# Optimization experiments

Hardware: AMD Instinct MI355X
Metric: run time of the kernel (lower is better)

Reference implementation:

```python
import jax, jax.numpy as jnp
import numpy as np

ENC_D, PRED_D, JOINT_D, VOCAB = 256, 256, 512, 1024

def setup_inputs() -> dict:
    key = jax.random.key(0)
    ks = jax.random.split(key, 8)
    B, T, U = 4, 256, 64
    s = lambda d: 1.0 / np.sqrt(d)
    return {
        "encoder_outputs": jax.random.normal(ks[0], (B, T, ENC_D), jnp.float32),
        "predictor_outputs": jax.random.normal(ks[1], (B, U, PRED_D), jnp.float32),
        "W_enc": jax.random.uniform(ks[2], (ENC_D, JOINT_D), jnp.float32, -s(ENC_D), s(ENC_D)),
        "b_enc": jax.random.uniform(ks[3], (JOINT_D,), jnp.float32, -s(ENC_D), s(ENC_D)),
        "W_dec": jax.random.uniform(ks[4], (PRED_D, JOINT_D), jnp.float32, -s(PRED_D), s(PRED_D)),
        "b_dec": jax.random.uniform(ks[5], (JOINT_D,), jnp.float32, -s(PRED_D), s(PRED_D)),
        "W_out": jax.random.uniform(ks[6], (JOINT_D, VOCAB), jnp.float32, -s(JOINT_D), s(JOINT_D)),
        "b_out": jax.random.uniform(ks[7], (VOCAB,), jnp.float32, -s(JOINT_D), s(JOINT_D)),
    }

def reference(encoder_outputs, predictor_outputs, W_enc, b_enc, W_dec, b_dec, W_out, b_out):
    # [B,T,J] and [B,U,J] projections
    enc = jnp.einsum('bte,ej->btj', encoder_outputs, W_enc) + b_enc
    pred = jnp.einsum('bup,pj->buj', predictor_outputs, W_dec) + b_dec
    # broadcast add -> [B,T,U,J], tanh, then output projection -> [B,T,U,V]
    joint = jnp.tanh(enc[:, :, None, :] + pred[:, None, :, :])
    logits = jnp.einsum('btuj,jv->btuv', joint, W_out) + b_out
    return logits
```

## Files before the change

kernel.cpp:

```cpp
#include <hip/hip_runtime.h>
#include <hip/hip_bf16.h>

typedef __attribute__((ext_vector_type(8))) short bf16x8;
typedef __attribute__((ext_vector_type(4))) float fvec4;
typedef __attribute__((ext_vector_type(16))) float f32x16;
typedef __attribute__((ext_vector_type(8))) unsigned short u16x8;


__device__ __forceinline__ unsigned short f2bf(float f) {
  unsigned int u = __builtin_bit_cast(unsigned int, f);
  u += 0x7FFFu + ((u >> 16) & 1u);
  return (unsigned short)(u >> 16);
}

__device__ __forceinline__ float fast_tanh(float x) {
  float cx = fminf(fmaxf(x, -9.0f), 9.0f);
  float e2 = __expf(cx + cx);
  return (e2 - 1.0f) * __builtin_amdgcn_rcpf(e2 + 1.0f);
}


__device__ __forceinline__ void proj_body(
    const float* __restrict__ x, const float* __restrict__ W,
    const float* __restrict__ bias, float* __restrict__ out,
    int blk, uint8_t* sh) {
  float (*xt)[9] = (float (*)[9])sh;
  const int tid = threadIdx.x;
  const int row0 = blk << 3;
  #pragma unroll
  for (int i = 0; i < 8; ++i)
    xt[tid][i] = x[(size_t)(row0 + i) * 256 + tid];
  __syncthreads();
  float acc0[8] = {0.f,0.f,0.f,0.f,0.f,0.f,0.f,0.f};
  float acc1[8] = {0.f,0.f,0.f,0.f,0.f,0.f,0.f,0.f};
  #pragma unroll 4
  for (int k = 0; k < 256; ++k) {
    float w0 = W[(size_t)k * 512 + tid];
    float w1 = W[(size_t)k * 512 + tid + 256];
    #pragma unroll
    for (int r = 0; r < 8; ++r) {
      float xv = xt[k][r];
      acc0[r] = fmaf(xv, w0, acc0[r]);
      acc1[r] = fmaf(xv, w1, acc1[r]);
    }
  }
  float b0 = bias[tid], b1 = bias[tid + 256];
  #pragma unroll
  for (int r = 0; r < 8; ++r) {
    out[(size_t)(row0 + r) * 512 + tid]       = acc0[r] + b0;
    out[(size_t)(row0 + r) * 512 + tid + 256] = acc1[r] + b1;
  }
}

__device__ __forceinline__ void transpose_body(
    const float* __restrict__ W, unsigned short* __restrict__ Bt3,
    int blk, uint8_t* sh) {
  unsigned short (*tile)[65] = (unsigned short (*)[65])sh;
  const int k0 = (blk & 7) << 6;
  const int n0 = (blk >> 3) << 6;
  const int tid = threadIdx.x;
  #pragma unroll
  for (int i = 0; i < 16; ++i) {
    int idx = tid + (i << 8);
    int r = idx >> 6, c = idx & 63;
    tile[r][c] = f2bf(W[(size_t)(k0 + r) * 1024 + n0 + c]);
  }
  __syncthreads();
  #pragma unroll
  for (int i = 0; i < 16; ++i) {
    int idx = tid + (i << 8);
    int r = idx >> 6, c = idx & 63;
    int ng = n0 + r, kg = k0 + c;
    size_t dst = ((size_t)(ng >> 9) << 18) + ((size_t)(kg >> 4) << 13)
               + ((ng & 511) << 4) + (kg & 15);
    Bt3[dst] = tile[c][r];
  }
}

__global__ __launch_bounds__(256) void prep_kernel(
    const float* __restrict__ enc, const float* __restrict__ We,
    const float* __restrict__ be, float* __restrict__ encp,
    const float* __restrict__ pred, const float* __restrict__ Wd,
    const float* __restrict__ bd, float* __restrict__ predp,
    const float* __restrict__ Wo, unsigned short* __restrict__ Bt3) {
  __shared__ uint8_t sh[9216];
  const int b = blockIdx.x;
  if (b < 128)       proj_body(enc, We, be, encp, b, sh);
  else if (b < 160)  proj_body(pred, Wd, bd, predp, b - 128, sh);
  else               transpose_body(Wo, Bt3, b - 160, sh);
}

__global__ __launch_bounds__(512, 4) void fused_gemm(
    const float* __restrict__ encp, const float* __restrict__ predp,
    const unsigned short* __restrict__ Bt3, const float* __restrict__ bout,
    float* __restrict__ out) {
  __shared__ uint8_t lds[66560];
  const int tid = threadIdx.x;
  const int lane = tid & 63, wid = tid >> 6;
  const int l31 = lane & 31, hi = lane >> 5;
  const int b = blockIdx.x;
  const int wg = ((b & 7) << 8) + (b >> 3);
  const int mt = wg >> 1, half = wg & 1;
  const int m0 = mt << 6;
  const int cb0 = half << 9;

  const unsigned short* Bgl =
      Bt3 + ((size_t)half << 18) + (((wid << 6) + l31) << 4) + (hi << 3);

  bf16x8 bA[2], bB[2];
  #pragma unroll
  for (int na = 0; na < 2; ++na)
    bA[na] = *(const bf16x8*)(Bgl + (na << 9));

  {
    const int r = tid >> 3, cb = tid & 7;
    const float* erow = encp + ((size_t)mt << 9);
    const float* prow = predp + ((size_t)(((mt >> 8) << 6) + r) << 9);
    uint8_t* rowbase = lds + (r << 10);
    #pragma unroll
    for (int c8 = 0; c8 < 8; ++c8) {
      int chunk = cb + (c8 << 3);
      int k8 = chunk << 3;
      fvec4 e0 = *(const fvec4*)(erow + k8);
      fvec4 e1 = *(const fvec4*)(erow + k8 + 4);
      fvec4 p0 = *(const fvec4*)(prow + k8);
      fvec4 p1 = *(const fvec4*)(prow + k8 + 4);
      u16x8 o;
      #pragma unroll
      for (int i = 0; i < 4; ++i) o[i]     = f2bf(fast_tanh(e0[i] + p0[i]));
      #pragma unroll
      for (int i = 0; i < 4; ++i) o[i + 4] = f2bf(fast_tanh(e1[i] + p1[i]));
      *(u16x8*)(rowbase + ((chunk ^ (r & 15)) << 4)) = o;
    }
  }
  asm volatile("s_waitcnt lgkmcnt(0)" ::: "memory");
  __builtin_amdgcn_s_barrier();

  f32x16 acc[2][2];
  #pragma unroll
  for (int i = 0; i < 2; ++i)
    #pragma unroll
    for (int j = 0; j < 2; ++j)
      #pragma unroll
      for (int e = 0; e < 16; ++e) acc[i][j][e] = 0.f;

  const int hx = hi ^ (lane & 15);
  int arowb[2];
  #pragma unroll
  for (int ma = 0; ma < 2; ++ma)
    arowb[ma] = ((ma << 5) + l31) << 10;

  auto step = [&](int kt, bf16x8 (&cur)[2], bf16x8 (&nxt)[2]) {
    const int ktn = kt < 31 ? kt + 1 : 31;
    #pragma unroll
    for (int na = 0; na < 2; ++na)
      nxt[na] = *(const bf16x8*)(Bgl + (ktn << 13) + (na << 9));
    const int ao = (((kt << 1) ^ hx) << 4);
    bf16x8 af[2];
    #pragma unroll
    for (int ma = 0; ma < 2; ++ma)
      af[ma] = *(const bf16x8*)(lds + arowb[ma] + ao);
    #pragma unroll
    for (int ma = 0; ma < 2; ++ma)
      #pragma unroll
      for (int na = 0; na < 2; ++na)
        acc[ma][na] = __builtin_amdgcn_mfma_f32_32x32x16_bf16(
            cur[na], af[ma], acc[ma][na], 0, 0, 0);
  };

  #pragma unroll
  for (int kt = 0; kt < 32; kt += 2) {
    step(kt,     bA, bB);
    step(kt + 1, bB, bA);
  }

  float (*epi)[516] = (float (*)[516])lds;
  fvec4 bvv[2][4];
  #pragma unroll
  for (int na = 0; na < 2; ++na)
    #pragma unroll
    for (int q = 0; q < 4; ++q)
      bvv[na][q] = *(const fvec4*)&bout[cb0 + (wid << 6) + (na << 5) +
                                       (q << 3) + (hi << 2)];

  #pragma unroll
  for (int ma = 0; ma < 2; ++ma) {
    asm volatile("s_waitcnt lgkmcnt(0)" ::: "memory");
    __builtin_amdgcn_s_barrier();
    #pragma unroll
    for (int na = 0; na < 2; ++na)
      #pragma unroll
      for (int q = 0; q < 4; ++q) {
        fvec4 o;
        #pragma unroll
        for (int j = 0; j < 4; ++j) o[j] = acc[ma][na][(q << 2) + j] + bvv[na][q][j];
        *(fvec4*)&epi[l31][(wid << 6) + (na << 5) + (q << 3) + (hi << 2)] = o;
      }
    asm volatile("s_waitcnt lgkmcnt(0)" ::: "memory");
    __builtin_amdgcn_s_barrier();
    #pragma unroll
    for (int j = 0; j < 8; ++j) {
      const int idx = (wid << 3) + j;
      const int row = idx >> 1, seg = idx & 1;
      fvec4 v = *(const fvec4*)&epi[row][(seg << 8) + (lane << 2)];
      const int gm = m0 + (ma << 5) + row;
      __builtin_nontemporal_store(
          v, (fvec4*)&out[(size_t)gm * 1024 + cb0 + (seg << 8) + (lane << 2)]);
    }
  }
}

extern "C" void kernel_launch(void* const* d_in, const int* in_sizes, int n_in,
                              void* d_out, int out_size, void* d_ws, size_t ws_size,
                              hipStream_t stream) {
  const float* enc   = (const float*)d_in[0];
  const float* pred  = (const float*)d_in[1];
  const float* W_enc = (const float*)d_in[2];
  const float* b_enc = (const float*)d_in[3];
  const float* W_dec = (const float*)d_in[4];
  const float* b_dec = (const float*)d_in[5];
  const float* W_out = (const float*)d_in[6];
  const float* b_out = (const float*)d_in[7];
  float* out = (float*)d_out;

  uint8_t* ws = (uint8_t*)d_ws;
  float* encp  = (float*)ws;
  float* predp = (float*)(ws + 2097152);
  unsigned short* bt3 = (unsigned short*)(ws + 2621440);

  prep_kernel<<<288, 256, 0, stream>>>(enc, W_enc, b_enc, encp,
                                       pred, W_dec, b_dec, predp,
                                       W_out, bt3);
  fused_gemm<<<2048, 512, 0, stream>>>(encp, predp, bt3, b_out, out);
}
```

Before: 126.3 us.

## Shrink GEMM tile to 64x128 and split A build into two K halves

Output tile per workgroup drops from 64x512 to 64x128, with each wave computing one 32x32 accumulator instead of a 2x2 set, and the grid grows from 2048 to 8192 blocks. The tanh-joint A tile is built in two K halves of 256 so LDS use falls to about 34KB, and launch bounds now ask for 8 blocks per CU. The aim is higher occupancy and lower register pressure to hide latency. The cost is rebuilding the joint tile once per 128-column tile, four times as often as before, plus less register reuse of B and A fragments and extra barriers.

```diff
diff --git a/kernel.cpp b/kernel.cpp
--- a/kernel.cpp
+++ b/kernel.cpp
@@ -90,35 +90,35 @@
   else               transpose_body(Wo, Bt3, b - 160, sh);
 }
 
-__global__ __launch_bounds__(512, 4) void fused_gemm(
+__global__ __launch_bounds__(512, 8) void fused_gemm(
     const float* __restrict__ encp, const float* __restrict__ predp,
     const unsigned short* __restrict__ Bt3, const float* __restrict__ bout,
     float* __restrict__ out) {
-  __shared__ uint8_t lds[66560];
+  __shared__ uint8_t lds[34816];
   const int tid = threadIdx.x;
   const int lane = tid & 63, wid = tid >> 6;
   const int l31 = lane & 31, hi = lane >> 5;
+  const int wm = wid >> 2, wn = wid & 3;
   const int b = blockIdx.x;
-  const int wg = ((b & 7) << 8) + (b >> 3);
-  const int mt = wg >> 1, half = wg & 1;
+  const int wg = ((b & 7) << 10) + (b >> 3);
+  const int mt = wg >> 3, nt = wg & 7;
   const int m0 = mt << 6;
-  const int cb0 = half << 9;
+  const int n0 = nt << 7;
+  const int half = nt >> 2;
 
   const unsigned short* Bgl =
-      Bt3 + ((size_t)half << 18) + (((wid << 6) + l31) << 4) + (hi << 3);
-
-  bf16x8 bA[2], bB[2];
-  #pragma unroll
-  for (int na = 0; na < 2; ++na)
-    bA[na] = *(const bf16x8*)(Bgl + (na << 9));
-
-  {
+      Bt3 + ((size_t)half << 18) + ((((nt & 3) << 7) + (wn << 5) + l31) << 4) + (hi << 3);
+
+  bf16x8 bA, bB;
+  bA = *(const bf16x8*)(Bgl);
+
+  auto build_A = [&](int h) {
     const int r = tid >> 3, cb = tid & 7;
-    const float* erow = encp + ((size_t)mt << 9);
-    const float* prow = predp + ((size_t)(((mt >> 8) << 6) + r) << 9);
-    uint8_t* rowbase = lds + (r << 10);
+    const float* erow = encp + ((size_t)mt << 9) + (h << 8);
+    const float* prow = predp + ((size_t)(((mt >> 8) << 6) + r) << 9) + (h << 8);
+    uint8_t* rowbase = lds + (r << 9);
     #pragma unroll
-    for (int c8 = 0; c8 < 8; ++c8) {
+    for (int c8 = 0; c8 < 4; ++c8) {
       int chunk = cb + (c8 << 3);
       int k8 = chunk << 3;
       fvec4 e0 = *(const fvec4*)(erow + k8);
@@ -132,81 +132,64 @@
       for (int i = 0; i < 4; ++i) o[i + 4] = f2bf(fast_tanh(e1[i] + p1[i]));
       *(u16x8*)(rowbase + ((chunk ^ (r & 15)) << 4)) = o;
     }
-  }
-  asm volatile("s_waitcnt lgkmcnt(0)" ::: "memory");
-  __builtin_amdgcn_s_barrier();
-
-  f32x16 acc[2][2];
-  #pragma unroll
-  for (int i = 0; i < 2; ++i)
-    #pragma unroll
-    for (int j = 0; j < 2; ++j)
-      #pragma unroll
-      for (int e = 0; e < 16; ++e) acc[i][j][e] = 0.f;
-
-  const int hx = hi ^ (lane & 15);
-  int arowb[2];
-  #pragma unroll
-  for (int ma = 0; ma < 2; ++ma)
-    arowb[ma] = ((ma << 5) + l31) << 10;
-
-  auto step = [&](int kt, bf16x8 (&cur)[2], bf16x8 (&nxt)[2]) {
+  };
+
+  build_A(0);
+  asm volatile("s_waitcnt lgkmcnt(0)" ::: "memory");
+  __builtin_amdgcn_s_barrier();
+
+  f32x16 acc;
+  #pragma unroll
+  for (int e = 0; e < 16; ++e) acc[e] = 0.f;
+
+  const int arow = (wm << 5) + l31;
+  const int abase = arow << 9;
+  const int am = arow & 15;
+
+  auto step = [&](int kt, bf16x8& cur, bf16x8& nxt) {
     const int ktn = kt < 31 ? kt + 1 : 31;
-    #pragma unroll
-    for (int na = 0; na < 2; ++na)
-      nxt[na] = *(const bf16x8*)(Bgl + (ktn << 13) + (na << 9));
-    const int ao = (((kt << 1) ^ hx) << 4);
-    bf16x8 af[2];
-    #pragma unroll
-    for (int ma = 0; ma < 2; ++ma)
-      af[ma] = *(const bf16x8*)(lds + arowb[ma] + ao);
-    #pragma unroll
-    for (int ma = 0; ma < 2; ++ma)
-      #pragma unroll
-      for (int na = 0; na < 2; ++na)
-        acc[ma][na] = __builtin_amdgcn_mfma_f32_32x32x16_bf16(
-            cur[na], af[ma], acc[ma][na], 0, 0, 0);
+    nxt = *(const bf16x8*)(Bgl + (ktn << 13));
+    const int ktl = kt & 15;
+    bf16x8 af = *(const bf16x8*)(lds + abase + ((((ktl << 1) | hi) ^ am) << 4));
+    acc = __builtin_amdgcn_mfma_f32_32x32x16_bf16(cur, af, acc, 0, 0, 0);
   };
 
   #pragma unroll
-  for (int kt = 0; kt < 32; kt += 2) {
+  for (int kt = 0; kt < 16; kt += 2) {
     step(kt,     bA, bB);
     step(kt + 1, bB, bA);
   }
-
-  float (*epi)[516] = (float (*)[516])lds;
-  fvec4 bvv[2][4];
-  #pragma unroll
-  for (int na = 0; na < 2; ++na)
+  asm volatile("s_waitcnt lgkmcnt(0)" ::: "memory");
+  __builtin_amdgcn_s_barrier();
+  build_A(1);
+  asm volatile("s_waitcnt lgkmcnt(0)" ::: "memory");
+  __builtin_amdgcn_s_barrier();
+  #pragma unroll
+  for (int kt = 16; kt < 32; kt += 2) {
+    step(kt,     bA, bB);
+    step(kt + 1, bB, bA);
+  }
+
+  float (*epi)[133] = (float (*)[133])lds;
+  asm volatile("s_waitcnt lgkmcnt(0)" ::: "memory");
+  __builtin_amdgcn_s_barrier();
+  #pragma unroll
+  for (int q = 0; q < 4; ++q) {
+    const int col = (wn << 5) + (q << 3) + (hi << 2);
+    fvec4 bv = *(const fvec4*)&bout[n0 + col];
+    fvec4 o;
     #pragma unroll
-    for (int q = 0; q < 4; ++q)
-      bvv[na][q] = *(const fvec4*)&bout[cb0 + (wid << 6) + (na << 5) +
-                                       (q << 3) + (hi << 2)];
-
-  #pragma unroll
-  for (int ma = 0; ma < 2; ++ma) {
-    asm volatile("s_waitcnt lgkmcnt(0)" ::: "memory");
-    __builtin_amdgcn_s_barrier();
-    #pragma unroll
-    for (int na = 0; na < 2; ++na)
-      #pragma unroll
-      for (int q = 0; q < 4; ++q) {
-        fvec4 o;
-        #pragma unroll
-        for (int j = 0; j < 4; ++j) o[j] = acc[ma][na][(q << 2) + j] + bvv[na][q][j];
-        *(fvec4*)&epi[l31][(wid << 6) + (na << 5) + (q << 3) + (hi << 2)] = o;
-      }
-    asm volatile("s_waitcnt lgkmcnt(0)" ::: "memory");
-    __builtin_amdgcn_s_barrier();
-    #pragma unroll
-    for (int j = 0; j < 8; ++j) {
-      const int idx = (wid << 3) + j;
-      const int row = idx >> 1, seg = idx & 1;
-      fvec4 v = *(const fvec4*)&epi[row][(seg << 8) + (lane << 2)];
-      const int gm = m0 + (ma << 5) + row;
-      __builtin_nontemporal_store(
-          v, (fvec4*)&out[(size_t)gm * 1024 + cb0 + (seg << 8) + (lane << 2)]);
-    }
+    for (int j = 0; j < 4; ++j) o[j] = acc[(q << 2) + j] + bv[j];
+    *(fvec4*)&epi[(wm << 5) + l31][col] = o;
+  }
+  asm volatile("s_waitcnt lgkmcnt(0)" ::: "memory");
+  __builtin_amdgcn_s_barrier();
+  #pragma unroll
+  for (int j = 0; j < 4; ++j) {
+    const int row = (wid << 3) + (j << 1) + hi;
+    fvec4 v = *(const fvec4*)&epi[row][l31 << 2];
+    __builtin_nontemporal_store(
+        v, (fvec4*)&out[(size_t)(m0 + row) * 1024 + n0 + (l31 << 2)]);
   }
 }
 
@@ -231,5 +214,5 @@
   prep_kernel<<<288, 256, 0, stream>>>(enc, W_enc, b_enc, encp,
                                        pred, W_dec, b_dec, predp,
                                        W_out, bt3);
-  fused_gemm<<<2048, 512, 0, stream>>>(encp, predp, bt3, b_out, out);
-}
+  fused_gemm<<<8192, 512, 0, stream>>>(encp, predp, bt3, b_out, out);
+}
```

After: 231.3 us. 83.1% more time.

## Split tanh joint computation into separate kernel writing bf16 A tiles

Applied to the files above, without the earlier changes.

Moves the broadcast-add, tanh and bf16 conversion out of the GEMM into a standalone joint_kernel that writes the full [B*T*U, 512] bf16 activation matrix to workspace in an MFMA-friendly layout. The GEMM then streams A fragments straight from global memory with register double-buffering instead of building them in LDS behind a barrier. This removes the duplicated tanh work (each A row was recomputed by both column halves) and the LDS prologue stall. In exchange it adds an extra launch and a large activation round trip through HBM (about 64 MB written and read back).

```diff
diff --git a/kernel.cpp b/kernel.cpp
--- a/kernel.cpp
+++ b/kernel.cpp
@@ -90,11 +90,38 @@
   else               transpose_body(Wo, Bt3, b - 160, sh);
 }
 
-__global__ __launch_bounds__(512, 4) void fused_gemm(
+__global__ __launch_bounds__(256) void joint_kernel(
     const float* __restrict__ encp, const float* __restrict__ predp,
-    const unsigned short* __restrict__ Bt3, const float* __restrict__ bout,
-    float* __restrict__ out) {
-  __shared__ uint8_t lds[66560];
+    unsigned short* __restrict__ Aj) {
+  const int vid = blockIdx.x * 256 + threadIdx.x;
+  const int r = vid & 31;
+  const int s = vid >> 5;
+  const int kt = s & 31;
+  const int g = s >> 5;
+  const int k0 = kt << 4;
+  const float* e = encp + ((size_t)(g >> 1) << 9) + k0;
+  const float* p = predp + (((size_t)((g >> 9) << 6) + ((g & 1) << 5) + r) << 9) + k0;
+  fvec4 ev0 = *(const fvec4*)e,        ev1 = *(const fvec4*)(e + 4);
+  fvec4 ev2 = *(const fvec4*)(e + 8),  ev3 = *(const fvec4*)(e + 12);
+  fvec4 pv0 = *(const fvec4*)p,        pv1 = *(const fvec4*)(p + 4);
+  fvec4 pv2 = *(const fvec4*)(p + 8),  pv3 = *(const fvec4*)(p + 12);
+  u16x8 o0, o1;
+  #pragma unroll
+  for (int i = 0; i < 4; ++i) {
+    o0[i]     = f2bf(fast_tanh(ev0[i] + pv0[i]));
+    o0[i + 4] = f2bf(fast_tanh(ev1[i] + pv1[i]));
+    o1[i]     = f2bf(fast_tanh(ev2[i] + pv2[i]));
+    o1[i + 4] = f2bf(fast_tanh(ev3[i] + pv3[i]));
+  }
+  unsigned short* dst = Aj + ((size_t)g << 14) + (kt << 9) + (r << 4);
+  *(u16x8*)dst = o0;
+  *(u16x8*)(dst + 8) = o1;
+}
+
+__global__ __launch_bounds__(512, 4) void gemm_kernel(
+    const unsigned short* __restrict__ Aj, const unsigned short* __restrict__ Bt3,
+    const float* __restrict__ bout, float* __restrict__ out) {
+  __shared__ uint8_t lds[66048];
   const int tid = threadIdx.x;
   const int lane = tid & 63, wid = tid >> 6;
   const int l31 = lane & 31, hi = lane >> 5;
@@ -106,35 +133,14 @@
 
   const unsigned short* Bgl =
       Bt3 + ((size_t)half << 18) + (((wid << 6) + l31) << 4) + (hi << 3);
-
-  bf16x8 bA[2], bB[2];
-  #pragma unroll
-  for (int na = 0; na < 2; ++na)
-    bA[na] = *(const bf16x8*)(Bgl + (na << 9));
-
-  {
-    const int r = tid >> 3, cb = tid & 7;
-    const float* erow = encp + ((size_t)mt << 9);
-    const float* prow = predp + ((size_t)(((mt >> 8) << 6) + r) << 9);
-    uint8_t* rowbase = lds + (r << 10);
-    #pragma unroll
-    for (int c8 = 0; c8 < 8; ++c8) {
-      int chunk = cb + (c8 << 3);
-      int k8 = chunk << 3;
-      fvec4 e0 = *(const fvec4*)(erow + k8);
-      fvec4 e1 = *(const fvec4*)(erow + k8 + 4);
-      fvec4 p0 = *(const fvec4*)(prow + k8);
-      fvec4 p1 = *(const fvec4*)(prow + k8 + 4);
-      u16x8 o;
-      #pragma unroll
-      for (int i = 0; i < 4; ++i) o[i]     = f2bf(fast_tanh(e0[i] + p0[i]));
-      #pragma unroll
-      for (int i = 0; i < 4; ++i) o[i + 4] = f2bf(fast_tanh(e1[i] + p1[i]));
-      *(u16x8*)(rowbase + ((chunk ^ (r & 15)) << 4)) = o;
-    }
-  }
-  asm volatile("s_waitcnt lgkmcnt(0)" ::: "memory");
-  __builtin_amdgcn_s_barrier();
+  const unsigned short* Agl =
+      Aj + ((size_t)mt << 15) + (l31 << 4) + (hi << 3);
+
+  bf16x8 bA[2], bB[2], aA[2], aB[2];
+  #pragma unroll
+  for (int na = 0; na < 2; ++na) bA[na] = *(const bf16x8*)(Bgl + (na << 9));
+  #pragma unroll
+  for (int ma = 0; ma < 2; ++ma) aA[ma] = *(const bf16x8*)(Agl + (ma << 14));
 
   f32x16 acc[2][2];
   #pragma unroll
@@ -144,34 +150,27 @@
       #pragma unroll
       for (int e = 0; e < 16; ++e) acc[i][j][e] = 0.f;
 
-  const int hx = hi ^ (lane & 15);
-  int arowb[2];
-  #pragma unroll
-  for (int ma = 0; ma < 2; ++ma)
-    arowb[ma] = ((ma << 5) + l31) << 10;
-
-  auto step = [&](int kt, bf16x8 (&cur)[2], bf16x8 (&nxt)[2]) {
+  auto step = [&](int kt, bf16x8 (&curB)[2], bf16x8 (&nxtB)[2],
+                  bf16x8 (&curA)[2], bf16x8 (&nxtA)[2]) {
     const int ktn = kt < 31 ? kt + 1 : 31;
     #pragma unroll
     for (int na = 0; na < 2; ++na)
-      nxt[na] = *(const bf16x8*)(Bgl + (ktn << 13) + (na << 9));
-    const int ao = (((kt << 1) ^ hx) << 4);
-    bf16x8 af[2];
+      nxtB[na] = *(const bf16x8*)(Bgl + (ktn << 13) + (na << 9));
     #pragma unroll
     for (int ma = 0; ma < 2; ++ma)
-      af[ma] = *(const bf16x8*)(lds + arowb[ma] + ao);
+      nxtA[ma] = *(const bf16x8*)(Agl + (ma << 14) + (ktn << 9));
     #pragma unroll
     for (int ma = 0; ma < 2; ++ma)
       #pragma unroll
       for (int na = 0; na < 2; ++na)
         acc[ma][na] = __builtin_amdgcn_mfma_f32_32x32x16_bf16(
-            cur[na], af[ma], acc[ma][na], 0, 0, 0);
+            curB[na], curA[ma], acc[ma][na], 0, 0, 0);
   };
 
   #pragma unroll
   for (int kt = 0; kt < 32; kt += 2) {
-    step(kt,     bA, bB);
-    step(kt + 1, bB, bA);
+    step(kt,     bA, bB, aA, aB);
+    step(kt + 1, bB, bA, aB, aA);
   }
 
   float (*epi)[516] = (float (*)[516])lds;
@@ -227,9 +226,11 @@
   float* encp  = (float*)ws;
   float* predp = (float*)(ws + 2097152);
   unsigned short* bt3 = (unsigned short*)(ws + 2621440);
+  unsigned short* aj  = (unsigned short*)(ws + 3670016);
 
   prep_kernel<<<288, 256, 0, stream>>>(enc, W_enc, b_enc, encp,
                                        pred, W_dec, b_dec, predp,
                                        W_out, bt3);
-  fused_gemm<<<2048, 512, 0, stream>>>(encp, predp, bt3, b_out, out);
-}
+  joint_kernel<<<8192, 256, 0, stream>>>(encp, predp, aj);
+  gemm_kernel<<<2048, 512, 0, stream>>>(aj, bt3, b_out, out);
+}
```

New measurement: 149.9 us. 1.19x slower.
